# Performance work log

Measured on AMD Instinct MI355X. Metric: run time of the kernel, lower is better.

The kernel has to match this reference:

```python
import jax, jax.numpy as jnp
from jax import lax
import numpy as np

NUM_ANCHORS = 3
NUM_CLASSES = 20
IMG_DIM = 416.0
ANCHORS = np.array([[10.0, 13.0], [16.0, 30.0], [33.0, 23.0]], dtype=np.float32)
BN_EPS = 1e-5


def setup_inputs() -> dict:
    key = jax.random.key(0)
    ks = jax.random.split(key, 8)
    B, Cin, G = 16, 256, 52
    Cmid = 2 * Cin
    Cout = NUM_ANCHORS * (NUM_CLASSES + 5)
    # weights scaled down so exp() in the box decode stays numerically tame
    return {
        "x": jax.random.normal(ks[0], (B, Cin, G, G), jnp.float32),
        "conv1_w": jax.random.normal(ks[1], (Cmid, Cin, 3, 3), jnp.float32) * 0.05,
        "bn_gamma": jnp.ones((Cmid,), jnp.float32),
        "bn_beta": jnp.zeros((Cmid,), jnp.float32),
        "bn_mean": jax.random.normal(ks[2], (Cmid,), jnp.float32) * 0.05,
        "bn_var": jax.random.uniform(ks[3], (Cmid,), jnp.float32, 0.5, 1.5),
        "conv2_w": jax.random.normal(ks[4], (Cout, Cmid, 1, 1), jnp.float32) * 0.05,
        "conv2_b": jnp.zeros((Cout,), jnp.float32),
    }


def _conv(x, w, padding):
    return lax.conv_general_dilated(
        x, w, window_strides=(1, 1), padding=padding,
        dimension_numbers=("NCHW", "OIHW", "NCHW"))


def reference(x, conv1_w, bn_gamma, bn_beta, bn_mean, bn_var, conv2_w, conv2_b):
    # BasicConv: conv3x3 (no bias) -> BatchNorm (inference stats) -> LeakyReLU(0.1)
    y = _conv(x, conv1_w, ((1, 1), (1, 1)))
    inv = bn_gamma / jnp.sqrt(bn_var + BN_EPS)
    y = y * inv[None, :, None, None] + (bn_beta - bn_mean * inv)[None, :, None, None]
    y = jnp.where(y > 0, y, 0.1 * y)
    # 1x1 head conv with bias
    y = _conv(y, conv2_w, ((0, 0), (0, 0))) + conv2_b[None, :, None, None]

    B, G = y.shape[0], y.shape[2]
    A, NC = NUM_ANCHORS, NUM_CLASSES
    # [B, A, 5+NC, G, G] -> [B, A, G, G, 5+NC]
    pred = y.reshape(B, A, NC + 5, G, G).transpose(0, 1, 3, 4, 2)

    obj_score = jax.nn.sigmoid(pred[..., 4])        # [B,A,G,G]
    pred_cls = jax.nn.sigmoid(pred[..., 5:])        # [B,A,G,G,NC]

    stride = IMG_DIM / G
    grid = jnp.arange(G, dtype=jnp.float32)
    grid_x = grid[None, None, None, :]              # [1,1,1,G]
    grid_y = grid[None, None, :, None]              # [1,1,G,1]
    scaled = jnp.asarray(ANCHORS) / stride          # [A,2]
    anchor_w = scaled[:, 0].reshape(1, A, 1, 1)
    anchor_h = scaled[:, 1].reshape(1, A, 1, 1)

    # original uses .data (detached) for box decode
    box_in = lax.stop_gradient(pred[..., :4])
    bx = jax.nn.sigmoid(box_in[..., 0]) + grid_x
    by = jax.nn.sigmoid(box_in[..., 1]) + grid_y
    bw = jnp.exp(box_in[..., 2]) * anchor_w
    bh = jnp.exp(box_in[..., 3]) * anchor_h
    pred_boxes = jnp.stack([bx, by, bw, bh], axis=-1) * stride  # [B,A,G,G,4]

    return jnp.concatenate(
        [pred_boxes.reshape(B, -1, 4),
         obj_score.reshape(B, -1, 1),
         pred_cls.reshape(B, -1, NC)], axis=-1)
```

## Files before the change

### kernel.cpp

```cpp
#include <hip/hip_runtime.h>

typedef _Float16 f16;
typedef _Float16 f16x8 __attribute__((ext_vector_type(8)));
typedef _Float16 f16x4 __attribute__((ext_vector_type(4)));
typedef float f32x4 __attribute__((ext_vector_type(4)));

#define GDIM 52
#define GG 2704
#define CIN 256
#define CMID 512
#define COUT 75
#define NIMG 16
#define SPT 192
#define NSPB 15
#define PH 60
#define PW 54

#define SLAB_SZ 24576

#define VMCNT0 asm volatile("s_waitcnt vmcnt(0)" ::: "memory")
#define SB0 __builtin_amdgcn_sched_barrier(0)

__device__ __forceinline__ float sigmoidf_(float x) {
    return 1.0f / (1.0f + __expf(-x));
}

__device__ __forceinline__ void gload16(const void* g, void* l) {
    __builtin_amdgcn_global_load_lds(
        (const __attribute__((address_space(1))) unsigned int*)g,
        (__attribute__((address_space(3))) unsigned int*)l, 16, 0, 0);
}

__global__ __launch_bounds__(256) void k_zero_border(f16* __restrict__ x16p) {
    int ic = blockIdx.x;
    int tid = threadIdx.x;
    f16x8 z;
#pragma unroll
    for (int k = 0; k < 8; ++k) z[k] = (f16)0;
    for (int j = tid; j < 536; j += 256) {
        int row, col;
        if (j < 432) { int r = j / 54; row = (r == 0) ? 0 : 52 + r; col = j % 54; }
        else { int k = j - 432; row = 1 + (k >> 1); col = (k & 1) * 53; }
        f16* p = x16p + (((size_t)ic * PH + row) * PW + col) * 32;
#pragma unroll
        for (int q = 0; q < 4; ++q) *(f16x8*)(p + q * 8) = z;
    }
}

__global__ __launch_bounds__(256) void k_prep_x(const float* __restrict__ x,
                                                f16* __restrict__ x16p) {
    __shared__ float ls[32][133];
    int hw0 = blockIdx.x * 128, ck = blockIdx.y, img = blockIdx.z;
    int tid = threadIdx.x;
    const float* xb = x + ((size_t)img * CIN + ck * 32) * GG;
#pragma unroll
    for (int i = 0; i < 16; ++i) {
        int idx = tid + i * 256;
        int r = idx >> 7, c = idx & 127;
        int hw = hw0 + c;
        ls[r][c] = (hw < GG) ? xb[(size_t)r * GG + hw] : 0.0f;
    }
    __syncthreads();
    int col = tid >> 1, half = tid & 1;
    int hw = hw0 + col;
    if (hw < GG) {
        int h = hw / GDIM, w = hw % GDIM;
        f16* dst = x16p + ((((size_t)img * 8 + ck) * PH + h + 1) * PW + (w + 1)) * 32 + half * 16;
        f16x8 o0, o1;
#pragma unroll
        for (int j = 0; j < 8; ++j) o0[j] = (f16)ls[half * 16 + j][col];
#pragma unroll
        for (int j = 0; j < 8; ++j) o1[j] = (f16)ls[half * 16 + 8 + j][col];
        *(f16x8*)dst = o0;
        *(f16x8*)(dst + 8) = o1;
    }
}

__global__ __launch_bounds__(256) void k_prep_w(
    const float* __restrict__ w1, const float* __restrict__ w2,
    const float* __restrict__ gamma, const float* __restrict__ beta,
    const float* __restrict__ mean, const float* __restrict__ var,
    f16* __restrict__ w16, f16* __restrict__ w2_16,
    float* __restrict__ bnscale, float* __restrict__ bnshift) {
    int i = blockIdx.x * 256 + threadIdx.x;
    int cl = i & 31;
    int co = (i >> 5) & 511;
    int ckt = i >> 14;
    int ck = ckt & 7, tap = ckt >> 3;
    int ci = ck * 32 + cl;
    w16[i] = (f16)w1[(size_t)co * 2304 + ci * 9 + tap];
    if (i < COUT * CMID) w2_16[i] = (f16)w2[i];
    if (i < CMID) {
        float s = gamma[i] * rsqrtf(var[i] + 1e-5f);
        bnscale[i] = s;
        bnshift[i] = beta[i] - mean[i] * s;
    }
}

#define TPX(T) ((((T) / 3 - 1) * PW + ((T) % 3) - 1) * 8)

__global__ __launch_bounds__(512, 2) void k_conv1(
    const f16* __restrict__ x16p, const f16* __restrict__ w16,
    const float* __restrict__ bnscale, const float* __restrict__ bnshift,
    f16* __restrict__ y16) {
    __shared__ __align__(16) char smem[101376];
    int img = blockIdx.x / NSPB, sb = blockIdx.x % NSPB;
    int n0 = sb * SPT;
    int h_lo = n0 / GDIM;
    int half = blockIdx.y;
    int co0 = half * 256;
    int tid = threadIdx.x;
    int lane = tid & 63, wave = tid >> 6;
    int wm = wave >> 1, wn = wave & 1;
    int l15 = lane & 15, kg = lane >> 4;
    int kgx = kg * 3072;

    int roff[6];
#pragma unroll
    for (int nf = 0; nf < 6; ++nf) {
        int n = n0 + wn * 96 + nf * 16 + l15;
        int nc = n < GG ? n : GG - 1;
        int hh = nc / GDIM, ww = nc % GDIM;
        roff[nf] = ((hh - h_lo + 1) * PW + (ww + 1)) * 8;
    }

    f32x4 acc[4][6];
#pragma unroll
    for (int a = 0; a < 4; ++a)
#pragma unroll
        for (int b = 0; b < 6; ++b) {
            acc[a][b][0] = 0.f; acc[a][b][1] = 0.f;
            acc[a][b][2] = 0.f; acc[a][b][3] = 0.f;
        }

    const f16* xbase = x16p + ((size_t)img * 8 * PH + h_lo) * (PW * 32);
    const f16* wAfrag = w16 + (size_t)co0 * 32 + (wm * 64 + l15) * 32 + kg * 8;

    {
        f16* sd = (f16*)smem;
#pragma unroll
        for (int p = 0; p < 3; ++p) {
            int c = p * 512 + tid;
            int s = c / 384, pix = c % 384;
            gload16(xbase + (size_t)pix * 32 + s * 8, sd + (size_t)c * 8);
        }
    }

    for (int ck = 0; ck < 8; ++ck) {
        VMCNT0;
        __builtin_amdgcn_s_barrier();
        SB0;
        if (ck < 7) {
            const f16* sg = xbase + (size_t)(ck + 1) * (PH * PW * 32);
            f16* sd = (f16*)(smem + ((ck + 1) & 1) * SLAB_SZ);
#pragma unroll
            for (int p = 0; p < 3; ++p) {
                int c = p * 512 + tid;
                int s = c / 384, pix = c % 384;
                gload16(sg + (size_t)pix * 32 + s * 8, sd + (size_t)c * 8);
            }
        }
        SB0;
        const f16* Sb = (const f16*)(smem + (ck & 1) * SLAB_SZ);
#pragma unroll
        for (int tap = 0; tap < 9; ++tap) {
            const f16* bp = Sb + kgx + TPX(tap);
            f16x8 b0 = *(const f16x8*)(bp + roff[0]);
            f16x8 b1 = *(const f16x8*)(bp + roff[1]);
            f16x8 b2 = *(const f16x8*)(bp + roff[2]);
            f16x8 b3 = *(const f16x8*)(bp + roff[3]);
            f16x8 b4 = *(const f16x8*)(bp + roff[4]);
            f16x8 b5 = *(const f16x8*)(bp + roff[5]);
            const f16* ap = wAfrag + (size_t)(tap * 8 + ck) * 16384;
            f16x8 a0 = *(const f16x8*)(ap);
            f16x8 a1 = *(const f16x8*)(ap + 512);
            f16x8 a2 = *(const f16x8*)(ap + 1024);
            f16x8 a3 = *(const f16x8*)(ap + 1536);
            __builtin_amdgcn_s_setprio(1);
#pragma unroll
            for (int nf = 0; nf < 6; ++nf) {
                f16x8 bf = nf == 0 ? b0 : nf == 1 ? b1 : nf == 2 ? b2
                         : nf == 3 ? b3 : nf == 4 ? b4 : b5;
                acc[0][nf] = __builtin_amdgcn_mfma_f32_16x16x32_f16(a0, bf, acc[0][nf], 0, 0, 0);
                acc[1][nf] = __builtin_amdgcn_mfma_f32_16x16x32_f16(a1, bf, acc[1][nf], 0, 0, 0);
                acc[2][nf] = __builtin_amdgcn_mfma_f32_16x16x32_f16(a2, bf, acc[2][nf], 0, 0, 0);
                acc[3][nf] = __builtin_amdgcn_mfma_f32_16x16x32_f16(a3, bf, acc[3][nf], 0, 0, 0);
            }
            __builtin_amdgcn_s_setprio(0);
            SB0;
        }
    }
    VMCNT0;
    __syncthreads();
    f16* tb = (f16*)smem;
#pragma unroll
    for (int mf = 0; mf < 4; ++mf) {
        int cr = wm * 64 + mf * 16 + kg * 4;
        f32x4 sc = *(const f32x4*)(bnscale + co0 + cr);
        f32x4 sh = *(const f32x4*)(bnshift + co0 + cr);
#pragma unroll
        for (int nf = 0; nf < 6; ++nf) {
            int pl = wn * 96 + nf * 16 + l15;
            f16x4 o;
#pragma unroll
            for (int i = 0; i < 4; ++i) {
                float v = acc[mf][nf][i] * sc[i] + sh[i];
                o[i] = (f16)(v > 0.f ? v : 0.1f * v);
            }
            *(f16x4*)(tb + pl * 264 + cr) = o;
        }
    }
    __syncthreads();
    int valid = GG - n0; if (valid > SPT) valid = SPT;
    f16* yb = y16 + (size_t)half * (NIMG * (size_t)GG * 256) + ((size_t)img * GG + n0) * 256;
#pragma unroll
    for (int p = 0; p < 12; ++p) {
        int u = p * 512 + tid, pl = u >> 5, slot = u & 31;
        if (pl < valid)
            *(f16x8*)(yb + (size_t)pl * 256 + slot * 8) =
                *(const f16x8*)(tb + pl * 264 + slot * 8);
    }
}

__global__ __launch_bounds__(256) void k_conv2(
    const f16* __restrict__ y16, const f16* __restrict__ w2_16,
    const float* __restrict__ b2, float* __restrict__ out) {
    __shared__ float ct[128][81];
    int img = blockIdx.x / 22, nb = blockIdx.x % 22;
    int n0 = nb * 128;
    int tid = threadIdx.x;
    int lane = tid & 63, wave = tid >> 6;
    int l15 = lane & 15, kg = lane >> 4;

    f32x4 acc[5][2];
#pragma unroll
    for (int a = 0; a < 5; ++a)
#pragma unroll
        for (int b = 0; b < 2; ++b) {
            acc[a][b][0] = 0.f; acc[a][b][1] = 0.f;
            acc[a][b][2] = 0.f; acc[a][b][3] = 0.f;
        }

    int nn[2];
#pragma unroll
    for (int nf = 0; nf < 2; ++nf) {
        int n = n0 + wave * 32 + nf * 16 + l15;
        nn[nf] = n < GG ? n : GG - 1;
    }
    for (int c0 = 0; c0 < CMID; c0 += 32) {
        const f16* yb = y16 + (size_t)(c0 >> 8) * (NIMG * (size_t)GG * 256) +
                        (size_t)img * GG * 256;
        int c = c0 & 255;
        f16x8 af[5];
#pragma unroll
        for (int mf = 0; mf < 5; ++mf) {
            int co = mf * 16 + l15;
            if (co < COUT)
                af[mf] = *(const f16x8*)(w2_16 + (size_t)co * CMID + c0 + kg * 8);
            else {
#pragma unroll
                for (int k = 0; k < 8; ++k) af[mf][k] = (f16)0;
            }
        }
#pragma unroll
        for (int nf = 0; nf < 2; ++nf) {
            f16x8 bf = *(const f16x8*)(yb + (size_t)nn[nf] * 256 + c + kg * 8);
#pragma unroll
            for (int mf = 0; mf < 5; ++mf)
                acc[mf][nf] = __builtin_amdgcn_mfma_f32_16x16x32_f16(
                    af[mf], bf, acc[mf][nf], 0, 0, 0);
        }
    }
#pragma unroll
    for (int mf = 0; mf < 5; ++mf)
#pragma unroll
        for (int nf = 0; nf < 2; ++nf)
            *(f32x4*)(&ct[wave * 32 + nf * 16 + l15][mf * 16 + kg * 4]) = acc[mf][nf];
    __syncthreads();
    for (int j = tid; j < 384; j += 256) {
        int a = j >> 7, nl = j & 127;
        int n = n0 + nl;
        if (n >= GG) continue;
        const float* t = &ct[nl][a * 25];
        float tv[25];
#pragma unroll
        for (int q = 0; q < 25; ++q) tv[q] = t[q] + b2[a * 25 + q];
        int h = n / GDIM, w = n % GDIM;
        const float AW[3] = {10.f, 16.f, 33.f};
        const float AH[3] = {13.f, 30.f, 23.f};
        float bx = (sigmoidf_(tv[0]) + (float)w) * 8.0f;
        float by = (sigmoidf_(tv[1]) + (float)h) * 8.0f;
        float bw_ = __expf(tv[2]) * AW[a];
        float bh_ = __expf(tv[3]) * AH[a];
        float* o = out + ((size_t)img * 8112 + (size_t)a * GG + n) * 25;
        o[0] = bx; o[1] = by; o[2] = bw_; o[3] = bh_;
        o[4] = sigmoidf_(tv[4]);
#pragma unroll
        for (int q = 0; q < 20; ++q) o[5 + q] = sigmoidf_(tv[5 + q]);
    }
}

extern "C" void kernel_launch(void* const* d_in, const int* in_sizes, int n_in,
                              void* d_out, int out_size, void* d_ws, size_t ws_size,
                              hipStream_t stream) {
    (void)in_sizes; (void)n_in; (void)out_size; (void)ws_size;
    const float* x     = (const float*)d_in[0];
    const float* w1    = (const float*)d_in[1];
    const float* gamma = (const float*)d_in[2];
    const float* beta  = (const float*)d_in[3];
    const float* mean  = (const float*)d_in[4];
    const float* var   = (const float*)d_in[5];
    const float* w2    = (const float*)d_in[6];
    const float* b2    = (const float*)d_in[7];
    float* out = (float*)d_out;

    char* ws = (char*)d_ws;
    f16* x16p     = (f16*)(ws);
    f16* w16      = (f16*)(ws + 26542080);
    f16* w2_16    = (f16*)(ws + 28901376);
    float* bnscale = (float*)(ws + 28978176);
    float* bnshift = (float*)(ws + 28980224);
    f16* y16      = (f16*)(ws + 28982272);

    k_zero_border<<<NIMG * 8, 256, 0, stream>>>(x16p);
    k_prep_x<<<dim3(22, 8, NIMG), 256, 0, stream>>>(x, x16p);
    k_prep_w<<<4608, 256, 0, stream>>>(w1, w2, gamma, beta, mean, var,
                                       w16, w2_16, bnscale, bnshift);
    k_conv1<<<dim3(NIMG * NSPB, 2), 512, 0, stream>>>(x16p, w16, bnscale,
                                                      bnshift, y16);
    k_conv2<<<NIMG * 22, 256, 0, stream>>>(y16, w2_16, b2, out);
}
```

Measured before the change: 160.0 us.

## Switch conv1 to 32x32x16 MFMA with 128-channel output tiles per block

After: 174.2 us. 8.9% more time.

```diff
diff --git a/kernel.cpp b/kernel.cpp
--- a/kernel.cpp
+++ b/kernel.cpp
@@ -4,6 +4,7 @@
 typedef _Float16 f16x8 __attribute__((ext_vector_type(8)));
 typedef _Float16 f16x4 __attribute__((ext_vector_type(4)));
 typedef float f32x4 __attribute__((ext_vector_type(4)));
+typedef float f32x16 __attribute__((ext_vector_type(16)));
 
 #define GDIM 52
 #define GG 2704
@@ -99,48 +100,46 @@
 
 #define TPX(T) ((((T) / 3 - 1) * PW + ((T) % 3) - 1) * 8)
 
-__global__ __launch_bounds__(512, 2) void k_conv1(
+__global__ __launch_bounds__(256, 3) void k_conv1(
     const f16* __restrict__ x16p, const f16* __restrict__ w16,
     const float* __restrict__ bnscale, const float* __restrict__ bnshift,
     f16* __restrict__ y16) {
-    __shared__ __align__(16) char smem[101376];
+    __shared__ __align__(16) char smem[50688];
     int img = blockIdx.x / NSPB, sb = blockIdx.x % NSPB;
     int n0 = sb * SPT;
     int h_lo = n0 / GDIM;
-    int half = blockIdx.y;
-    int co0 = half * 256;
+    int quarter = blockIdx.y;
+    int co0 = quarter * 128;
     int tid = threadIdx.x;
     int lane = tid & 63, wave = tid >> 6;
     int wm = wave >> 1, wn = wave & 1;
-    int l15 = lane & 15, kg = lane >> 4;
-    int kgx = kg * 3072;
-
-    int roff[6];
-#pragma unroll
-    for (int nf = 0; nf < 6; ++nf) {
-        int n = n0 + wn * 96 + nf * 16 + l15;
+    int l31 = lane & 31, hi = lane >> 5;
+
+    int roff[3];
+#pragma unroll
+    for (int nt = 0; nt < 3; ++nt) {
+        int n = n0 + wn * 96 + nt * 32 + l31;
         int nc = n < GG ? n : GG - 1;
         int hh = nc / GDIM, ww = nc % GDIM;
-        roff[nf] = ((hh - h_lo + 1) * PW + (ww + 1)) * 8;
-    }
-
-    f32x4 acc[4][6];
-#pragma unroll
-    for (int a = 0; a < 4; ++a)
-#pragma unroll
-        for (int b = 0; b < 6; ++b) {
-            acc[a][b][0] = 0.f; acc[a][b][1] = 0.f;
-            acc[a][b][2] = 0.f; acc[a][b][3] = 0.f;
-        }
+        roff[nt] = ((hh - h_lo + 1) * PW + (ww + 1)) * 8;
+    }
+
+    f32x16 acc[2][3];
+#pragma unroll
+    for (int a = 0; a < 2; ++a)
+#pragma unroll
+        for (int b = 0; b < 3; ++b)
+#pragma unroll
+            for (int i = 0; i < 16; ++i) acc[a][b][i] = 0.f;
 
     const f16* xbase = x16p + ((size_t)img * 8 * PH + h_lo) * (PW * 32);
-    const f16* wAfrag = w16 + (size_t)co0 * 32 + (wm * 64 + l15) * 32 + kg * 8;
+    const f16* wAfrag = w16 + ((size_t)co0 + wm * 64 + l31) * 32 + hi * 8;
 
     {
         f16* sd = (f16*)smem;
 #pragma unroll
-        for (int p = 0; p < 3; ++p) {
-            int c = p * 512 + tid;
+        for (int p = 0; p < 6; ++p) {
+            int c = p * 256 + tid;
             int s = c / 384, pix = c % 384;
             gload16(xbase + (size_t)pix * 32 + s * 8, sd + (size_t)c * 8);
         }
@@ -154,8 +153,8 @@
             const f16* sg = xbase + (size_t)(ck + 1) * (PH * PW * 32);
             f16* sd = (f16*)(smem + ((ck + 1) & 1) * SLAB_SZ);
 #pragma unroll
-            for (int p = 0; p < 3; ++p) {
-                int c = p * 512 + tid;
+            for (int p = 0; p < 6; ++p) {
+                int c = p * 256 + tid;
                 int s = c / 384, pix = c % 384;
                 gload16(sg + (size_t)pix * 32 + s * 8, sd + (size_t)c * 8);
             }
@@ -164,29 +163,39 @@
         const f16* Sb = (const f16*)(smem + (ck & 1) * SLAB_SZ);
 #pragma unroll
         for (int tap = 0; tap < 9; ++tap) {
-            const f16* bp = Sb + kgx + TPX(tap);
-            f16x8 b0 = *(const f16x8*)(bp + roff[0]);
-            f16x8 b1 = *(const f16x8*)(bp + roff[1]);
-            f16x8 b2 = *(const f16x8*)(bp + roff[2]);
-            f16x8 b3 = *(const f16x8*)(bp + roff[3]);
-            f16x8 b4 = *(const f16x8*)(bp + roff[4]);
-            f16x8 b5 = *(const f16x8*)(bp + roff[5]);
             const f16* ap = wAfrag + (size_t)(tap * 8 + ck) * 16384;
-            f16x8 a0 = *(const f16x8*)(ap);
-            f16x8 a1 = *(const f16x8*)(ap + 512);
-            f16x8 a2 = *(const f16x8*)(ap + 1024);
-            f16x8 a3 = *(const f16x8*)(ap + 1536);
-            __builtin_amdgcn_s_setprio(1);
-#pragma unroll
-            for (int nf = 0; nf < 6; ++nf) {
-                f16x8 bf = nf == 0 ? b0 : nf == 1 ? b1 : nf == 2 ? b2
-                         : nf == 3 ? b3 : nf == 4 ? b4 : b5;
-                acc[0][nf] = __builtin_amdgcn_mfma_f32_16x16x32_f16(a0, bf, acc[0][nf], 0, 0, 0);
-                acc[1][nf] = __builtin_amdgcn_mfma_f32_16x16x32_f16(a1, bf, acc[1][nf], 0, 0, 0);
-                acc[2][nf] = __builtin_amdgcn_mfma_f32_16x16x32_f16(a2, bf, acc[2][nf], 0, 0, 0);
-                acc[3][nf] = __builtin_amdgcn_mfma_f32_16x16x32_f16(a3, bf, acc[3][nf], 0, 0, 0);
-            }
-            __builtin_amdgcn_s_setprio(0);
+            const f16* bp0 = Sb + hi * 3072 + TPX(tap);
+            const f16* bp1 = Sb + (2 + hi) * 3072 + TPX(tap);
+            {
+                f16x8 b0 = *(const f16x8*)(bp0 + roff[0]);
+                f16x8 b1 = *(const f16x8*)(bp0 + roff[1]);
+                f16x8 b2 = *(const f16x8*)(bp0 + roff[2]);
+                f16x8 a0 = *(const f16x8*)(ap);
+                f16x8 a1 = *(const f16x8*)(ap + 1024);
+                __builtin_amdgcn_s_setprio(1);
+                acc[0][0] = __builtin_amdgcn_mfma_f32_32x32x16_f16(a0, b0, acc[0][0], 0, 0, 0);
+                acc[1][0] = __builtin_amdgcn_mfma_f32_32x32x16_f16(a1, b0, acc[1][0], 0, 0, 0);
+                acc[0][1] = __builtin_amdgcn_mfma_f32_32x32x16_f16(a0, b1, acc[0][1], 0, 0, 0);
+                acc[1][1] = __builtin_amdgcn_mfma_f32_32x32x16_f16(a1, b1, acc[1][1], 0, 0, 0);
+                acc[0][2] = __builtin_amdgcn_mfma_f32_32x32x16_f16(a0, b2, acc[0][2], 0, 0, 0);
+                acc[1][2] = __builtin_amdgcn_mfma_f32_32x32x16_f16(a1, b2, acc[1][2], 0, 0, 0);
+                __builtin_amdgcn_s_setprio(0);
+            }
+            {
+                f16x8 b0 = *(const f16x8*)(bp1 + roff[0]);
+                f16x8 b1 = *(const f16x8*)(bp1 + roff[1]);
+                f16x8 b2 = *(const f16x8*)(bp1 + roff[2]);
+                f16x8 a0 = *(const f16x8*)(ap + 16);
+                f16x8 a1 = *(const f16x8*)(ap + 1040);
+                __builtin_amdgcn_s_setprio(1);
+                acc[0][0] = __builtin_amdgcn_mfma_f32_32x32x16_f16(a0, b0, acc[0][0], 0, 0, 0);
+                acc[1][0] = __builtin_amdgcn_mfma_f32_32x32x16_f16(a1, b0, acc[1][0], 0, 0, 0);
+                acc[0][1] = __builtin_amdgcn_mfma_f32_32x32x16_f16(a0, b1, acc[0][1], 0, 0, 0);
+                acc[1][1] = __builtin_amdgcn_mfma_f32_32x32x16_f16(a1, b1, acc[1][1], 0, 0, 0);
+                acc[0][2] = __builtin_amdgcn_mfma_f32_32x32x16_f16(a0, b2, acc[0][2], 0, 0, 0);
+                acc[1][2] = __builtin_amdgcn_mfma_f32_32x32x16_f16(a1, b2, acc[1][2], 0, 0, 0);
+                __builtin_amdgcn_s_setprio(0);
+            }
             SB0;
         }
     }
@@ -194,31 +203,34 @@
     __syncthreads();
     f16* tb = (f16*)smem;
 #pragma unroll
-    for (int mf = 0; mf < 4; ++mf) {
-        int cr = wm * 64 + mf * 16 + kg * 4;
-        f32x4 sc = *(const f32x4*)(bnscale + co0 + cr);
-        f32x4 sh = *(const f32x4*)(bnshift + co0 + cr);
-#pragma unroll
-        for (int nf = 0; nf < 6; ++nf) {
-            int pl = wn * 96 + nf * 16 + l15;
-            f16x4 o;
-#pragma unroll
-            for (int i = 0; i < 4; ++i) {
-                float v = acc[mf][nf][i] * sc[i] + sh[i];
-                o[i] = (f16)(v > 0.f ? v : 0.1f * v);
-            }
-            *(f16x4*)(tb + pl * 264 + cr) = o;
-        }
-    }
+    for (int mt = 0; mt < 2; ++mt)
+#pragma unroll
+        for (int q = 0; q < 4; ++q) {
+            int co_l = wm * 64 + mt * 32 + q * 8 + hi * 4;
+            f32x4 sc = *(const f32x4*)(bnscale + co0 + co_l);
+            f32x4 sh = *(const f32x4*)(bnshift + co0 + co_l);
+#pragma unroll
+            for (int nt = 0; nt < 3; ++nt) {
+                int pix_l = wn * 96 + nt * 32 + l31;
+                f16x4 o;
+#pragma unroll
+                for (int i = 0; i < 4; ++i) {
+                    float v = acc[mt][nt][q * 4 + i] * sc[i] + sh[i];
+                    o[i] = (f16)(v > 0.f ? v : 0.1f * v);
+                }
+                *(f16x4*)(tb + pix_l * 132 + co_l) = o;
+            }
+        }
     __syncthreads();
     int valid = GG - n0; if (valid > SPT) valid = SPT;
-    f16* yb = y16 + (size_t)half * (NIMG * (size_t)GG * 256) + ((size_t)img * GG + n0) * 256;
+    f16* yb = y16 + (size_t)quarter * (NIMG * (size_t)GG * 128) +
+              ((size_t)img * GG + n0) * 128;
 #pragma unroll
     for (int p = 0; p < 12; ++p) {
-        int u = p * 512 + tid, pl = u >> 5, slot = u & 31;
+        int u = p * 256 + tid, pl = u >> 4, slot = u & 15;
         if (pl < valid)
-            *(f16x8*)(yb + (size_t)pl * 256 + slot * 8) =
-                *(const f16x8*)(tb + pl * 264 + slot * 8);
+            *(f16x8*)(yb + (size_t)pl * 128 + slot * 8) =
+                *(const f16x8*)(tb + pl * 132 + slot * 8);
     }
 }
 
@@ -248,9 +260,9 @@
         nn[nf] = n < GG ? n : GG - 1;
     }
     for (int c0 = 0; c0 < CMID; c0 += 32) {
-        const f16* yb = y16 + (size_t)(c0 >> 8) * (NIMG * (size_t)GG * 256) +
-                        (size_t)img * GG * 256;
-        int c = c0 & 255;
+        const f16* yb = y16 + (size_t)(c0 >> 7) * (NIMG * (size_t)GG * 128) +
+                        (size_t)img * GG * 128;
+        int c = c0 & 127;
         f16x8 af[5];
 #pragma unroll
         for (int mf = 0; mf < 5; ++mf) {
@@ -264,7 +276,7 @@
         }
 #pragma unroll
         for (int nf = 0; nf < 2; ++nf) {
-            f16x8 bf = *(const f16x8*)(yb + (size_t)nn[nf] * 256 + c + kg * 8);
+            f16x8 bf = *(const f16x8*)(yb + (size_t)nn[nf] * 128 + c + kg * 8);
 #pragma unroll
             for (int mf = 0; mf < 5; ++mf)
                 acc[mf][nf] = __builtin_amdgcn_mfma_f32_16x16x32_f16(
@@ -326,7 +338,7 @@
     k_prep_x<<<dim3(22, 8, NIMG), 256, 0, stream>>>(x, x16p);
     k_prep_w<<<4608, 256, 0, stream>>>(w1, w2, gamma, beta, mean, var,
                                        w16, w2_16, bnscale, bnshift);
-    k_conv1<<<dim3(NIMG * NSPB, 2), 512, 0, stream>>>(x16p, w16, bnscale,
+    k_conv1<<<dim3(NIMG * NSPB, 4), 256, 0, stream>>>(x16p, w16, bnscale,
                                                       bnshift, y16);
     k_conv2<<<NIMG * 22, 256, 0, stream>>>(y16, w2_16, b2, out);
 }
```
